# Kernel tuning notes

Hardware: AMD Instinct MI355X
Metric: run time of the kernel (lower is better)

Reference implementation:

```python
import jax, jax.numpy as jnp
import numpy as np

L, D, H, DFF = 4, 1024, 16, 4096
DH = D // H
B, T = 2, 2048
EPS = 1e-5


def setup_inputs() -> dict:
    key = jax.random.key(0)
    ks = jax.random.split(key, 16)
    xav_a = (6.0 / (D + D)) ** 0.5      # xavier_uniform for square DxD
    xav_f1 = (6.0 / (D + DFF)) ** 0.5
    xav_f2 = (6.0 / (DFF + D)) ** 0.5
    def u(k, shape, a):
        return jax.random.uniform(k, shape, jnp.float32, -a, a)
    inp = {
        "x": jax.random.normal(ks[0], (B, T, D), jnp.float32),
        "mask": jnp.ones((B, T), jnp.int32),
        # attention projections, torch Linear layout [out, in]
        "Wq": u(ks[1], (L, D, D), xav_a), "bq": jnp.zeros((L, D), jnp.float32),
        "Wk": u(ks[2], (L, D, D), xav_a), "bk": jnp.zeros((L, D), jnp.float32),
        "Wv": u(ks[3], (L, D, D), xav_a), "bv": jnp.zeros((L, D), jnp.float32),
        "Wo": u(ks[4], (L, D, D), xav_a), "bo": jnp.zeros((L, D), jnp.float32),
        # FFN
        "fc1_w": u(ks[5], (L, DFF, D), xav_f1), "fc1_b": jnp.zeros((L, DFF), jnp.float32),
        "fc2_w": u(ks[6], (L, D, DFF), xav_f2), "fc2_b": jnp.zeros((L, D), jnp.float32),
        # LayerNorms
        "ln1_g": jnp.ones((L, D), jnp.float32), "ln1_b": jnp.zeros((L, D), jnp.float32),
        "ln2_g": jnp.ones((L, D), jnp.float32), "ln2_b": jnp.zeros((L, D), jnp.float32),
        "lnf_g": jnp.ones((D,), jnp.float32), "lnf_b": jnp.zeros((D,), jnp.float32),
    }
    return inp


def _layernorm(x, g, b):
    mu = jnp.mean(x, axis=-1, keepdims=True)
    var = jnp.mean(jnp.square(x - mu), axis=-1, keepdims=True)
    return (x - mu) * jax.lax.rsqrt(var + EPS) * g + b


def _encoder_forward(x, mask, Wq, bq, Wk, bk, Wv, bv, Wo, bo,
                     fc1_w, fc1_b, fc2_w, fc2_b,
                     ln1_g, ln1_b, ln2_g, ln2_b, lnf_g, lnf_b):
    keep = mask.astype(bool)[:, None, None, :]  # [B,1,1,Tk]
    scale = 1.0 / (DH ** 0.5)
    for l in range(L):
        # --- multi-head self-attention ---
        q = (jnp.einsum('btd,ed->bte', x, Wq[l]) + bq[l]).reshape(B, T, H, DH).transpose(0, 2, 1, 3)
        k = (jnp.einsum('btd,ed->bte', x, Wk[l]) + bk[l]).reshape(B, T, H, DH).transpose(0, 2, 1, 3)
        v = (jnp.einsum('btd,ed->bte', x, Wv[l]) + bv[l]).reshape(B, T, H, DH).transpose(0, 2, 1, 3)
        logits = jnp.einsum('bhqd,bhkd->bhqk', q, k) * scale
        logits = jnp.where(keep, logits, -jnp.inf)
        attn = jax.nn.softmax(logits, axis=-1)
        ctx = jnp.einsum('bhqk,bhkd->bhqd', attn, v).transpose(0, 2, 1, 3).reshape(B, T, D)
        attn_out = jnp.einsum('btd,ed->bte', ctx, Wo[l]) + bo[l]
        x = _layernorm(x + attn_out, ln1_g[l], ln1_b[l])
        # --- feed-forward (exact GELU, like torch nn.GELU default) ---
        h = jax.nn.gelu(jnp.einsum('btd,fd->btf', x, fc1_w[l]) + fc1_b[l], approximate=False)
        ff_out = jnp.einsum('btf,df->btd', h, fc2_w[l]) + fc2_b[l]
        x = _layernorm(x + ff_out, ln2_g[l], ln2_b[l])
    return _layernorm(x, lnf_g, lnf_b)


def reference(x, mask, Wq, bq, Wk, bk, Wv, bv, Wo, bo,
              fc1_w, fc1_b, fc2_w, fc2_b,
              ln1_g, ln1_b, ln2_g, ln2_b, lnf_g, lnf_b):
    return _encoder_forward(x, mask, Wq, bq, Wk, bk, Wv, bv, Wo, bo,
                            fc1_w, fc1_b, fc2_w, fc2_b,
                            ln1_g, ln1_b, ln2_g, ln2_b, lnf_g, lnf_b)
```

## Files before the change

kernel.cpp:

```cpp
#include <hip/hip_runtime.h>
#include <hip/hip_bf16.h>
#include <cstdint>

#define BB 2
#define TT 2048
#define DD 1024
#define HH 16
#define DHH 64
#define DFF 4096
#define LL 4
#define MM (BB*TT)
#define NT (TT/64)

typedef __attribute__((ext_vector_type(8))) short short8v;
typedef __attribute__((ext_vector_type(4))) short short4v;
typedef __attribute__((ext_vector_type(4))) float floatx4;

typedef __attribute__((address_space(3))) void lds_void;
typedef const __attribute__((address_space(1))) void glb_void;

__device__ __forceinline__ void gload_lds16(const void* g, void* l) {
  __builtin_amdgcn_global_load_lds((glb_void*)g, (lds_void*)l, 16, 0, 0);
}

__device__ __forceinline__ float bf2f(short s) {
  union { unsigned u; float f; } v; v.u = ((unsigned)(unsigned short)s) << 16; return v.f;
}
__device__ __forceinline__ short f2bf(float f) {
  union { float f; unsigned u; } v; v.f = f;
  unsigned r = (v.u + 0x7fffu + ((v.u >> 16) & 1u)) >> 16;
  return (short)r;
}
__device__ __forceinline__ unsigned pack2bf(float a, float b) {
  __hip_bfloat162 h = __float22bfloat162_rn(make_float2(a, b));
  return *reinterpret_cast<unsigned*>(&h);
}
__device__ __forceinline__ float fexp2(float x) {
  float r; asm("v_exp_f32 %0, %1" : "=v"(r) : "v"(x)); return r;
}
__device__ __forceinline__ float max3f(float a, float b, float c) {
  float r; asm("v_max3_f32 %0, %1, %2, %3" : "=v"(r) : "v"(a), "v"(b), "v"(c)); return r;
}
__device__ __forceinline__ float gelu_fast(float x) {
  const float u = x * x;
  const float w = fmaf(u, -0.10294537f, -2.302203f);
  const float t = fexp2(w * x);
  return x * __builtin_amdgcn_rcpf(1.f + t);
}

#define SCL2 0.18033688011112042f
__device__ __forceinline__ short8v scale8(short8v v) {
  short8v r;
#pragma unroll
  for (int i = 0; i < 8; ++i) r[i] = f2bf(bf2f(v[i]) * SCL2);
  return r;
}

#define SEG (DD*DD)
#define WTOT (4*SEG + 2*DFF*DD)
__global__ __launch_bounds__(256) void cast_layer(
    const float* __restrict__ wq, const float* __restrict__ wk,
    const float* __restrict__ wv, const float* __restrict__ wo,
    const float* __restrict__ f1, const float* __restrict__ f2,
    short* __restrict__ dst)
{
  const int i = (blockIdx.x * 256 + threadIdx.x) * 4;
  const float* src; int off;
  if      (i <     SEG) { src = wq; off = i; }
  else if (i < 2 * SEG) { src = wk; off = i - SEG; }
  else if (i < 3 * SEG) { src = wv; off = i - 2 * SEG; }
  else if (i < 4 * SEG) { src = wo; off = i - 3 * SEG; }
  else if (i < 4 * SEG + DFF * DD) { src = f1; off = i - 4 * SEG; }
  else { src = f2; off = i - 4 * SEG - DFF * DD; }
  const float4 v = *(const float4*)(src + off);
  short4v o; o[0] = f2bf(v.x); o[1] = f2bf(v.y); o[2] = f2bf(v.z); o[3] = f2bf(v.w);
  *(short4v*)(dst + i) = o;
}

__global__ __launch_bounds__(256) void concat_bias(
    const float* __restrict__ a, const float* __restrict__ b,
    const float* __restrict__ c, float* __restrict__ o)
{
  const int i = blockIdx.x * 256 + threadIdx.x;
  o[i] = i < DD ? a[i] : (i < 2 * DD ? b[i - DD] : c[i - 2 * DD]);
}

template<int GELU>
__global__ __launch_bounds__(512, 2) void gemm256(
    const short* __restrict__ A, const short* __restrict__ W,
    const float* __restrict__ bias, short* __restrict__ C,
    int M, int N, int K)
{
  __shared__ __align__(16) short lds[65536];
  const int t = threadIdx.x;
  const int lane = t & 63, wave = t >> 6;
  const int wm = wave >> 2, wn = wave & 3;
  const int l15 = lane & 15, lg = lane >> 4;

  const int nwg = gridDim.x * gridDim.y;
  const int bid0 = blockIdx.y * gridDim.x + blockIdx.x;
  const int q8 = nwg >> 3;
  const int lid = (bid0 & 7) * q8 + (bid0 >> 3);
  const int bx = lid % gridDim.x, by = lid / gridDim.x;

  const size_t abase = (size_t)by * 256 * K;
  const size_t wbase = (size_t)bx * 256 * K;

  floatx4 acc[8][4];
  floatx4 zero = {0.f, 0.f, 0.f, 0.f};
#pragma unroll
  for (int m = 0; m < 8; ++m)
#pragma unroll
    for (int n = 0; n < 4; ++n) acc[m][n] = zero;

#define STG_A(sl_, h_, u_) do {                                                \
    _Pragma("unroll")                                                          \
    for (int j_ = 0; j_ < 2; ++j_) {                                           \
      const int c_ = j_ * 512 + t, r_ = c_ >> 3;                               \
      const int kc_ = (c_ & 7) ^ (r_ & 7);                                     \
      gload_lds16(A + abase + (size_t)((h_) * 128 + r_) * K + (u_) * 64 + kc_ * 8, \
                  &lds[(sl_) * 16384 + (h_) * 8192 + (j_ * 512 + wave * 64) * 8]); \
    } } while (0)
#define STG_B(sl_, h_, u_) do {                                                \
    _Pragma("unroll")                                                          \
    for (int j_ = 0; j_ < 2; ++j_) {                                           \
      const int c_ = j_ * 512 + t, r_ = c_ >> 3;                               \
      const int kc_ = (c_ & 7) ^ (r_ & 7);                                     \
      gload_lds16(W + wbase + (size_t)((h_) * 128 + r_) * K + (u_) * 64 + kc_ * 8, \
                  &lds[32768 + (sl_) * 16384 + (h_) * 8192 + (j_ * 512 + wave * 64) * 8]); \
    } } while (0)

  const int NTK = K >> 6;
  STG_A(0, 0, 0); STG_A(0, 1, 0); STG_B(0, 0, 0); STG_B(0, 1, 0);

  for (int u = 0; u < NTK; ++u) {
    const int sl = u & 1, ns = sl ^ 1;
    const int aoff = sl * 16384 + wm * 8192;
    const int boff = 32768 + sl * 16384 + (wn >> 1) * 8192;
    short8v bfr[4][2];
#pragma unroll
    for (int p = 0; p < 4; ++p) {
      if (p == 0) {
        if (u + 1 < NTK) {
          STG_A(ns, 0, u + 1);
          asm volatile("s_waitcnt vmcnt(2)" ::: "memory");
        } else {
          asm volatile("s_waitcnt vmcnt(0)" ::: "memory");
        }
        __builtin_amdgcn_s_barrier();
#pragma unroll
        for (int n = 0; n < 4; ++n)
#pragma unroll
          for (int kk = 0; kk < 2; ++kk) {
            const int rl = (wn & 1) * 64 + n * 16 + l15;
            bfr[n][kk] = *(const short8v*)&lds[boff + rl * 64 + ((kk * 4 + lg) ^ (rl & 7)) * 8];
          }
      } else if (p == 1) { if (u + 1 < NTK) STG_A(ns, 1, u + 1); }
      else if (p == 2)   { if (u + 1 < NTK) STG_B(ns, 0, u + 1); }
      else               { if (u + 1 < NTK) STG_B(ns, 1, u + 1); }

      short8v af[2][2];
#pragma unroll
      for (int i = 0; i < 2; ++i)
#pragma unroll
        for (int kk = 0; kk < 2; ++kk) {
          const int rl = (2 * p + i) * 16 + l15;
          af[i][kk] = *(const short8v*)&lds[aoff + rl * 64 + ((kk * 4 + lg) ^ (rl & 7)) * 8];
        }
      asm volatile("s_waitcnt lgkmcnt(0)" ::: "memory");
      __builtin_amdgcn_s_setprio(1);
#pragma unroll
      for (int kk = 0; kk < 2; ++kk)
#pragma unroll
        for (int i = 0; i < 2; ++i)
#pragma unroll
          for (int n = 0; n < 4; ++n)
            acc[2 * p + i][n] = __builtin_amdgcn_mfma_f32_16x16x32_bf16(
                af[i][kk], bfr[n][kk], acc[2 * p + i][n], 0, 0, 0);
      __builtin_amdgcn_s_setprio(0);
      __builtin_amdgcn_s_barrier();
    }
  }
#undef STG_A
#undef STG_B

  float bv[4];
#pragma unroll
  for (int n = 0; n < 4; ++n)
    bv[n] = bias[bx * 256 + wn * 64 + n * 16 + l15];
#pragma unroll
  for (int m = 0; m < 8; ++m)
#pragma unroll
    for (int jj = 0; jj < 4; ++jj) {
      const int row = by * 256 + wm * 128 + m * 16 + lg * 4 + jj;
      short* cp = C + (size_t)row * N + bx * 256 + wn * 64 + l15;
#pragma unroll
      for (int n = 0; n < 4; ++n) {
        float v = acc[m][n][jj] + bv[n];
        if (GELU) v = gelu_fast(v);
        cp[n * 16] = f2bf(v);
      }
    }
}

template<int GELU>
__global__ __launch_bounds__(512, 2) void gemm128(
    const short* __restrict__ A, const short* __restrict__ W,
    const float* __restrict__ bias, short* __restrict__ C,
    int M, int N, int K)
{
  __shared__ __align__(16) short lds[32768];
  const int t = threadIdx.x;
  const int lane = t & 63, wave = t >> 6;
  const int wm = wave >> 2, wn = wave & 3;
  const int l15 = lane & 15, lg = lane >> 4;

  const int nwg = gridDim.x * gridDim.y;
  const int bid0 = blockIdx.y * gridDim.x + blockIdx.x;
  const int q8 = nwg >> 3;
  const int lid = (bid0 & 7) * q8 + (bid0 >> 3);
  const int bx = lid % gridDim.x, by = lid / gridDim.x;

  const size_t abase = (size_t)by * 128 * K;
  const size_t wbase = (size_t)bx * 128 * K;

  floatx4 acc[4][2];
  floatx4 zero = {0.f, 0.f, 0.f, 0.f};
#pragma unroll
  for (int m = 0; m < 4; ++m)
#pragma unroll
    for (int n = 0; n < 2; ++n) acc[m][n] = zero;

#define STG_A(sl_, u_) do {                                                    \
    _Pragma("unroll")                                                          \
    for (int j_ = 0; j_ < 2; ++j_) {                                           \
      const int c_ = j_ * 512 + t, r_ = c_ >> 3;                               \
      const int kc_ = (c_ & 7) ^ (r_ & 7);                                     \
      gload_lds16(A + abase + (size_t)r_ * K + (u_) * 64 + kc_ * 8,            \
                  &lds[(sl_) * 8192 + (j_ * 512 + wave * 64) * 8]);            \
    } } while (0)
#define STG_B(sl_, u_) do {                                                    \
    _Pragma("unroll")                                                          \
    for (int j_ = 0; j_ < 2; ++j_) {                                           \
      const int c_ = j_ * 512 + t, r_ = c_ >> 3;                               \
      const int kc_ = (c_ & 7) ^ (r_ & 7);                                     \
      gload_lds16(W + wbase + (size_t)r_ * K + (u_) * 64 + kc_ * 8,            \
                  &lds[16384 + (sl_) * 8192 + (j_ * 512 + wave * 64) * 8]);    \
    } } while (0)

  const int NTK = K >> 6;
  STG_A(0, 0); STG_B(0, 0);

  for (int u = 0; u < NTK; ++u) {
    const int sl = u & 1, ns = sl ^ 1;
    if (u + 1 < NTK) {
      STG_A(ns, u + 1);
      asm volatile("s_waitcnt vmcnt(2)" ::: "memory");
    } else {
      asm volatile("s_waitcnt vmcnt(0)" ::: "memory");
    }
    __builtin_amdgcn_s_barrier();

    short8v bfr[2][2];
#pragma unroll
    for (int n = 0; n < 2; ++n)
#pragma unroll
      for (int kk = 0; kk < 2; ++kk) {
        const int rl = wn * 32 + n * 16 + l15;
        bfr[n][kk] = *(const short8v*)&lds[16384 + sl * 8192 + rl * 64 + ((kk * 4 + lg) ^ (rl & 7)) * 8];
      }
    short8v af0[2][2];
#pragma unroll
    for (int m = 0; m < 2; ++m)
#pragma unroll
      for (int kk = 0; kk < 2; ++kk) {
        const int rl = wm * 64 + m * 16 + l15;
        af0[m][kk] = *(const short8v*)&lds[sl * 8192 + rl * 64 + ((kk * 4 + lg) ^ (rl & 7)) * 8];
      }
    asm volatile("s_waitcnt lgkmcnt(0)" ::: "memory");
    __builtin_amdgcn_s_setprio(1);
#pragma unroll
    for (int kk = 0; kk < 2; ++kk)
#pragma unroll
      for (int m = 0; m < 2; ++m)
#pragma unroll
        for (int n = 0; n < 2; ++n)
          acc[m][n] = __builtin_amdgcn_mfma_f32_16x16x32_bf16(af0[m][kk], bfr[n][kk], acc[m][n], 0, 0, 0);
    __builtin_amdgcn_s_setprio(0);

    if (u + 1 < NTK) STG_B(ns, u + 1);
    short8v af1[2][2];
#pragma unroll
    for (int m = 0; m < 2; ++m)
#pragma unroll
      for (int kk = 0; kk < 2; ++kk) {
        const int rl = wm * 64 + (2 + m) * 16 + l15;
        af1[m][kk] = *(const short8v*)&lds[sl * 8192 + rl * 64 + ((kk * 4 + lg) ^ (rl & 7)) * 8];
      }
    asm volatile("s_waitcnt lgkmcnt(0)" ::: "memory");
    __builtin_amdgcn_s_setprio(1);
#pragma unroll
    for (int kk = 0; kk < 2; ++kk)
#pragma unroll
      for (int m = 0; m < 2; ++m)
#pragma unroll
        for (int n = 0; n < 2; ++n)
          acc[2 + m][n] = __builtin_amdgcn_mfma_f32_16x16x32_bf16(af1[m][kk], bfr[n][kk], acc[2 + m][n], 0, 0, 0);
    __builtin_amdgcn_s_setprio(0);
    __builtin_amdgcn_s_barrier();
  }
#undef STG_A
#undef STG_B

  float bv[2];
#pragma unroll
  for (int n = 0; n < 2; ++n)
    bv[n] = bias[bx * 128 + wn * 32 + n * 16 + l15];
#pragma unroll
  for (int m = 0; m < 4; ++m)
#pragma unroll
    for (int jj = 0; jj < 4; ++jj) {
      const int row = by * 128 + wm * 64 + m * 16 + lg * 4 + jj;
      short* cp = C + (size_t)row * N + bx * 128 + wn * 32 + l15;
#pragma unroll
      for (int n = 0; n < 2; ++n) {
        float v = acc[m][n][jj] + bv[n];
        if (GELU) v = gelu_fast(v);
        cp[n * 16] = f2bf(v);
      }
    }
}

__global__ __launch_bounds__(256) void transpose_v(
    const short* __restrict__ qkv, short* __restrict__ vt)
{
  __shared__ short tile[64][65];
  const int tb = blockIdx.x, h = blockIdx.y, b = blockIdx.z;
  const int t = threadIdx.x;
  const int r = t >> 2, c4 = (t & 3) * 16;
  const short* src = qkv + ((size_t)(b * TT + tb * 64 + r)) * 3072 + 2048 + h * 64 + c4;
#pragma unroll
  for (int i = 0; i < 16; ++i) tile[r][c4 + i] = src[i];
  __syncthreads();
  short* dst = vt + ((size_t)((b * HH + h) * 64 + r)) * TT + tb * 64 + c4;
#pragma unroll
  for (int i = 0; i < 16; ++i) dst[i] = tile[c4 + i][r];
}

#define PSTR 72
__global__ __launch_bounds__(512, 4) void flash_attn(
    const short* __restrict__ qkv, const short* __restrict__ vt,
    const int* __restrict__ mask, short* __restrict__ ctx)
{
  const int t = threadIdx.x;
  const int lane = t & 63, wave = t >> 6;
  const int l15 = lane & 15, lg = lane >> 4;

  const int bid0 = blockIdx.x + gridDim.x * (blockIdx.y + gridDim.y * blockIdx.z);
  const int lid = (bid0 & 7) * 64 + (bid0 >> 3);
  const int qb = lid & 15, h = (lid >> 4) & 15, b = lid >> 8;

  __shared__ __align__(16) short Ks[2][64 * 64];
  __shared__ __align__(16) short Vs[2][64 * 64];
  __shared__ __align__(16) short p_lds[8][16 * PSTR];
  short* prow = p_lds[wave];

  const short* qp = qkv + ((size_t)(b * TT + qb * 128 + wave * 16 + l15)) * 3072 + h * 64;
  const short8v qf0 = scale8(*(const short8v*)(qp + lg * 8));
  const short8v qf1 = scale8(*(const short8v*)(qp + 32 + lg * 8));

  const short* kbase = qkv + (size_t)b * TT * 3072 + 1024 + h * 64;
  const short* vtb   = vt + ((size_t)(b * HH + h)) * 64 * TT;

  const int srow = lane >> 3;
  const int scol = (lane & 7) ^ (srow & 7);

  float m_run = -3e30f, l_run = 0.f;
  floatx4 zero = {0.f, 0.f, 0.f, 0.f};
  floatx4 o[4];
#pragma unroll
  for (int n = 0; n < 4; ++n) o[n] = zero;

#define STAGE_KV(bufi, kb_) do {                                             \
    const int r_ = wave * 8 + srow;                                          \
    gload_lds16(kbase + (size_t)((kb_) * 64 + r_) * 3072 + scol * 8,         \
                &Ks[bufi][wave * 512]);                                      \
    gload_lds16(vtb + (size_t)r_ * TT + (kb_) * 64 + scol * 8,               \
                &Vs[bufi][wave * 512]);                                      \
  } while (0)

  STAGE_KV(0, 0);
  int buf = 0;
  for (int kb = 0; kb < NT; ++kb) {
    if (kb + 1 < NT) {
      STAGE_KV(buf ^ 1, kb + 1);
      asm volatile("s_waitcnt vmcnt(2)" ::: "memory");
    } else {
      asm volatile("s_waitcnt vmcnt(0)" ::: "memory");
    }
    __builtin_amdgcn_s_barrier();

    float cm[4][4];
#pragma unroll
    for (int n = 0; n < 4; ++n) {
      const int4 mv = *(const int4*)&mask[b * TT + kb * 64 + n * 16 + lg * 4];
      cm[n][0] = mv.x ? 0.f : -1.5e30f; cm[n][1] = mv.y ? 0.f : -1.5e30f;
      cm[n][2] = mv.z ? 0.f : -1.5e30f; cm[n][3] = mv.w ? 0.f : -1.5e30f;
    }

    floatx4 s[4];
#pragma unroll
    for (int n = 0; n < 4; ++n) {
      const int row = n * 16 + l15;
      const int ch0 = lg ^ (row & 7);
      const int ch1 = (lg + 4) ^ (row & 7);
      const short8v kf0 = *(const short8v*)&Ks[buf][row * 64 + ch0 * 8];
      const short8v kf1 = *(const short8v*)&Ks[buf][row * 64 + ch1 * 8];
      floatx4 a = zero;
      a = __builtin_amdgcn_mfma_f32_16x16x32_bf16(kf0, qf0, a, 0, 0, 0);
      a = __builtin_amdgcn_mfma_f32_16x16x32_bf16(kf1, qf1, a, 0, 0, 0);
      s[n] = a;
    }
#pragma unroll
    for (int n = 0; n < 4; ++n)
#pragma unroll
      for (int jj = 0; jj < 4; ++jj) s[n][jj] += cm[n][jj];

    const float t0 = max3f(s[0][0], s[0][1], s[0][2]);
    const float t1 = max3f(s[0][3], s[1][0], s[1][1]);
    const float t2 = max3f(s[1][2], s[1][3], s[2][0]);
    const float t3 = max3f(s[2][1], s[2][2], s[2][3]);
    const float t4 = max3f(s[3][0], s[3][1], s[3][2]);
    float mx = fmaxf(max3f(t0, t1, t2), max3f(t3, t4, s[3][3]));
    mx = fmaxf(mx, __shfl_xor(mx, 16, 64));
    mx = fmaxf(mx, __shfl_xor(mx, 32, 64));

    const bool defer = __all(mx - m_run <= 11.5f);
    const float mnew = defer ? m_run : fmaxf(m_run, mx);
    float ps[4];
#pragma unroll
    for (int n = 0; n < 4; ++n) {
      s[n][0] = fexp2(s[n][0] - mnew);
      s[n][1] = fexp2(s[n][1] - mnew);
      s[n][2] = fexp2(s[n][2] - mnew);
      s[n][3] = fexp2(s[n][3] - mnew);
      ps[n] = (s[n][0] + s[n][1]) + (s[n][2] + s[n][3]);
    }
    float sum = (ps[0] + ps[1]) + (ps[2] + ps[3]);
    sum += __shfl_xor(sum, 16, 64);
    sum += __shfl_xor(sum, 32, 64);
    if (defer) {
      l_run += sum;
    } else {
      const float al = fexp2(m_run - mnew);
      l_run = l_run * al + sum;
      m_run = mnew;
      float alo[4];
#pragma unroll
      for (int jj = 0; jj < 4; ++jj) alo[jj] = __shfl(al, lg * 4 + jj, 16);
#pragma unroll
      for (int n = 0; n < 4; ++n)
#pragma unroll
        for (int jj = 0; jj < 4; ++jj) o[n][jj] *= alo[jj];
    }

#pragma unroll
    for (int n = 0; n < 4; ++n) {
      const unsigned u0 = pack2bf(s[n][0], s[n][1]);
      const unsigned u1 = pack2bf(s[n][2], s[n][3]);
      *(uint2*)&prow[l15 * PSTR + n * 16 + lg * 4] = make_uint2(u0, u1);
    }
    const short8v pf0 = *(const short8v*)&prow[l15 * PSTR + lg * 8];
    const short8v pf1 = *(const short8v*)&prow[l15 * PSTR + 32 + lg * 8];

#pragma unroll
    for (int n = 0; n < 4; ++n) {
      const int row = n * 16 + l15;
      const int ch0 = lg ^ (row & 7);
      const int ch1 = (lg + 4) ^ (row & 7);
      const short8v vf0 = *(const short8v*)&Vs[buf][row * 64 + ch0 * 8];
      const short8v vf1 = *(const short8v*)&Vs[buf][row * 64 + ch1 * 8];
      o[n] = __builtin_amdgcn_mfma_f32_16x16x32_bf16(pf0, vf0, o[n], 0, 0, 0);
      o[n] = __builtin_amdgcn_mfma_f32_16x16x32_bf16(pf1, vf1, o[n], 0, 0, 0);
    }
    asm volatile("" ::: "memory");
    __builtin_amdgcn_s_barrier();
    buf ^= 1;
  }
#undef STAGE_KV

#pragma unroll
  for (int jj = 0; jj < 4; ++jj) {
    const float inv = 1.f / __shfl(l_run, lg * 4 + jj, 16);
    const int row = qb * 128 + wave * 16 + lg * 4 + jj;
#pragma unroll
    for (int n = 0; n < 4; ++n)
      ctx[((size_t)(b * TT + row)) * DD + h * 64 + n * 16 + l15] = f2bf(o[n][jj] * inv);
  }
}

__global__ __launch_bounds__(256) void add_ln(
    const float* __restrict__ xres, const short* __restrict__ add,
    const float* __restrict__ g, const float* __restrict__ bb,
    float* __restrict__ outf, short* __restrict__ outb)
{
  const int row = blockIdx.x, t = threadIdx.x;
  const int lane = t & 63, wave = t >> 6;
  const float4 xv = *(const float4*)(xres + (size_t)row * DD + t * 4);
  float y[4] = { xv.x, xv.y, xv.z, xv.w };
  if (add) {
    const short4v av = *(const short4v*)(add + (size_t)row * DD + t * 4);
#pragma unroll
    for (int i = 0; i < 4; ++i) y[i] += bf2f(av[i]);
  }
  float s = y[0] + y[1] + y[2] + y[3];
  float ss = y[0]*y[0] + y[1]*y[1] + y[2]*y[2] + y[3]*y[3];
#pragma unroll
  for (int off = 32; off >= 1; off >>= 1) {
    s  += __shfl_xor(s, off, 64);
    ss += __shfl_xor(ss, off, 64);
  }
  __shared__ float red[2][4];
  if (lane == 0) { red[0][wave] = s; red[1][wave] = ss; }
  __syncthreads();
  s  = red[0][0] + red[0][1] + red[0][2] + red[0][3];
  ss = red[1][0] + red[1][1] + red[1][2] + red[1][3];
  const float mu = s * (1.f / DD);
  const float var = ss * (1.f / DD) - mu * mu;
  const float rs = rsqrtf(var + 1e-5f);
  const float4 gv = *(const float4*)(g + t * 4);
  const float4 bv = *(const float4*)(bb + t * 4);
  float o[4];
  o[0] = (y[0] - mu) * rs * gv.x + bv.x;
  o[1] = (y[1] - mu) * rs * gv.y + bv.y;
  o[2] = (y[2] - mu) * rs * gv.z + bv.z;
  o[3] = (y[3] - mu) * rs * gv.w + bv.w;
  if (outf) *(float4*)(outf + (size_t)row * DD + t * 4) = make_float4(o[0], o[1], o[2], o[3]);
  if (outb) {
    short4v ov;
#pragma unroll
    for (int i = 0; i < 4; ++i) ov[i] = f2bf(o[i]);
    *(short4v*)(outb + (size_t)row * DD + t * 4) = ov;
  }
}

__global__ __launch_bounds__(256) void cast_in(
    const float* __restrict__ x, float* __restrict__ xf,
    short* __restrict__ xb)
{
  const int i = (blockIdx.x * 256 + threadIdx.x) * 4;
  const float4 v = *(const float4*)(x + i);
  *(float4*)(xf + i) = v;
  short4v o; o[0] = f2bf(v.x); o[1] = f2bf(v.y); o[2] = f2bf(v.z); o[3] = f2bf(v.w);
  *(short4v*)(xb + i) = o;
}

extern "C" void kernel_launch(void* const* d_in, const int* in_sizes, int n_in,
                              void* d_out, int out_size, void* d_ws, size_t ws_size,
                              hipStream_t stream) {
  const float* x   = (const float*)d_in[0];
  const int* mask  = (const int*)d_in[1];
  const float* Wq  = (const float*)d_in[2];
  const float* bq  = (const float*)d_in[3];
  const float* Wk  = (const float*)d_in[4];
  const float* bk  = (const float*)d_in[5];
  const float* Wv  = (const float*)d_in[6];
  const float* bv  = (const float*)d_in[7];
  const float* Wo  = (const float*)d_in[8];
  const float* bo  = (const float*)d_in[9];
  const float* f1w = (const float*)d_in[10];
  const float* f1b = (const float*)d_in[11];
  const float* f2w = (const float*)d_in[12];
  const float* f2b = (const float*)d_in[13];
  const float* l1g = (const float*)d_in[14];
  const float* l1b = (const float*)d_in[15];
  const float* l2g = (const float*)d_in[16];
  const float* l2b = (const float*)d_in[17];
  const float* lfg = (const float*)d_in[18];
  const float* lfb = (const float*)d_in[19];
  float* out = (float*)d_out;

  char* ws = (char*)d_ws;
  const size_t MB = 1u << 20;
  float* xf   = (float*)(ws);
  short* xb   = (short*)(ws + 16 * MB);
  short* qkv  = (short*)(ws + 24 * MB);
  short* vt_  = (short*)(ws + 48 * MB);
  short* ctx  = (short*)(ws + 56 * MB);
  short* tmp  = (short*)(ws + 64 * MB);
  float* fbias= (float*)(ws + 64 * MB);
  short* wbuf = (short*)(ws + 72 * MB);
  short* hb   = qkv;

  cast_in<<<(MM * DD) / (256 * 4), 256, 0, stream>>>(x, xf, xb);

  for (int l = 0; l < LL; ++l) {
    cast_layer<<<WTOT / (256 * 4), 256, 0, stream>>>(
        Wq + (size_t)l * SEG, Wk + (size_t)l * SEG, Wv + (size_t)l * SEG, Wo + (size_t)l * SEG,
        f1w + (size_t)l * DFF * DD, f2w + (size_t)l * DD * DFF, wbuf);
    concat_bias<<<12, 256, 0, stream>>>(bq + l * DD, bk + l * DD, bv + l * DD, fbias);
    const short* wqkv_b = wbuf;
    const short* wo_b   = wbuf + 3 * SEG;
    const short* f1_b   = wbuf + 4 * SEG;
    const short* f2_b   = wbuf + 4 * SEG + DFF * DD;

    gemm256<0><<<dim3(3072 / 256, MM / 256), 512, 0, stream>>>(xb, wqkv_b, fbias, qkv, MM, 3072, DD);
    transpose_v<<<dim3(TT / 64, HH, BB), 256, 0, stream>>>(qkv, vt_);
    flash_attn<<<dim3(TT / 128, HH, BB), 512, 0, stream>>>(qkv, vt_, mask, ctx);
    gemm128<0><<<dim3(DD / 128, MM / 128), 512, 0, stream>>>(ctx, wo_b, bo + l * DD, tmp, MM, DD, DD);
    add_ln<<<MM, 256, 0, stream>>>(xf, tmp, l1g + l * DD, l1b + l * DD, xf, xb);
    gemm256<1><<<dim3(DFF / 256, MM / 256), 512, 0, stream>>>(xb, f1_b, f1b + l * DFF, hb, MM, DFF, DD);
    gemm128<0><<<dim3(DD / 128, MM / 128), 512, 0, stream>>>(hb, f2_b, f2b + l * DD, tmp, MM, DD, DFF);
    add_ln<<<MM, 256, 0, stream>>>(xf, tmp, l2g + l * DD, l2b + l * DD, xf, xb);
  }
  add_ln<<<MM, 256, 0, stream>>>(xf, nullptr, lfg, lfb, out, nullptr);
}
```

Measured before the change: 958.0 us.

## Triple-buffer gemm128 and flash-attn K/V staging; fold QKV bias concat into GEMM

The 128-tile GEMM and the flash-attention K/V loop move from double to triple LDS buffering. Loads run two tiles ahead, the trailing barrier per iteration is removed, and A and W for a tile are staged together. The QKV GEMM now picks among the three bias vectors by column segment, so the concat_bias launch per layer is gone. This trades more LDS per block, which may lower occupancy, for better overlap of global loads with MFMA work and fewer barriers.

```diff
diff --git a/kernel.cpp b/kernel.cpp
--- a/kernel.cpp
+++ b/kernel.cpp
@@ -77,18 +77,11 @@
   *(short4v*)(dst + i) = o;
 }
 
-__global__ __launch_bounds__(256) void concat_bias(
-    const float* __restrict__ a, const float* __restrict__ b,
-    const float* __restrict__ c, float* __restrict__ o)
-{
-  const int i = blockIdx.x * 256 + threadIdx.x;
-  o[i] = i < DD ? a[i] : (i < 2 * DD ? b[i - DD] : c[i - 2 * DD]);
-}
-
-template<int GELU>
+template<int GELU, int QKV>
 __global__ __launch_bounds__(512, 2) void gemm256(
     const short* __restrict__ A, const short* __restrict__ W,
-    const float* __restrict__ bias, short* __restrict__ C,
+    const float* __restrict__ b0, const float* __restrict__ b1,
+    const float* __restrict__ b2, short* __restrict__ C,
     int M, int N, int K)
 {
   __shared__ __align__(16) short lds[65536];
@@ -184,10 +177,19 @@
 #undef STG_A
 #undef STG_B
 
+  const float* bp;
+  int cbase = bx * 256 + wn * 64;
+  if (QKV) {
+    const int seg = cbase >> 10;
+    bp = (seg == 0) ? b0 : (seg == 1 ? b1 : b2);
+    cbase -= seg << 10;
+  } else {
+    bp = b0;
+  }
   float bv[4];
 #pragma unroll
   for (int n = 0; n < 4; ++n)
-    bv[n] = bias[bx * 256 + wn * 64 + n * 16 + l15];
+    bv[n] = bp[cbase + n * 16 + l15];
 #pragma unroll
   for (int m = 0; m < 8; ++m)
 #pragma unroll
@@ -209,7 +211,7 @@
     const float* __restrict__ bias, short* __restrict__ C,
     int M, int N, int K)
 {
-  __shared__ __align__(16) short lds[32768];
+  __shared__ __align__(16) short lds[49152];
   const int t = threadIdx.x;
   const int lane = t & 63, wave = t >> 6;
   const int wm = wave >> 2, wn = wave & 3;
@@ -231,86 +233,55 @@
 #pragma unroll
     for (int n = 0; n < 2; ++n) acc[m][n] = zero;
 
-#define STG_A(sl_, u_) do {                                                    \
+#define STG128(sl_, u_) do {                                                   \
     _Pragma("unroll")                                                          \
     for (int j_ = 0; j_ < 2; ++j_) {                                           \
       const int c_ = j_ * 512 + t, r_ = c_ >> 3;                               \
       const int kc_ = (c_ & 7) ^ (r_ & 7);                                     \
       gload_lds16(A + abase + (size_t)r_ * K + (u_) * 64 + kc_ * 8,            \
                   &lds[(sl_) * 8192 + (j_ * 512 + wave * 64) * 8]);            \
+      gload_lds16(W + wbase + (size_t)r_ * K + (u_) * 64 + kc_ * 8,            \
+                  &lds[24576 + (sl_) * 8192 + (j_ * 512 + wave * 64) * 8]);    \
     } } while (0)
-#define STG_B(sl_, u_) do {                                                    \
-    _Pragma("unroll")                                                          \
-    for (int j_ = 0; j_ < 2; ++j_) {                                           \
-      const int c_ = j_ * 512 + t, r_ = c_ >> 3;                               \
-      const int kc_ = (c_ & 7) ^ (r_ & 7);                                     \
-      gload_lds16(W + wbase + (size_t)r_ * K + (u_) * 64 + kc_ * 8,            \
-                  &lds[16384 + (sl_) * 8192 + (j_ * 512 + wave * 64) * 8]);    \
-    } } while (0)
 
   const int NTK = K >> 6;
-  STG_A(0, 0); STG_B(0, 0);
+  STG128(0, 0);
+  STG128(1, 1);
 
   for (int u = 0; u < NTK; ++u) {
-    const int sl = u & 1, ns = sl ^ 1;
-    if (u + 1 < NTK) {
-      STG_A(ns, u + 1);
-      asm volatile("s_waitcnt vmcnt(2)" ::: "memory");
-    } else {
-      asm volatile("s_waitcnt vmcnt(0)" ::: "memory");
-    }
+    const int sl = u % 3;
+    if (u + 1 < NTK) asm volatile("s_waitcnt vmcnt(4)" ::: "memory");
+    else             asm volatile("s_waitcnt vmcnt(0)" ::: "memory");
     __builtin_amdgcn_s_barrier();
-
-    short8v bfr[2][2];
+    if (u + 2 < NTK) STG128((u + 2) % 3, u + 2);
+
+    short8v bfr[2][2], af[4][2];
 #pragma unroll
     for (int n = 0; n < 2; ++n)
 #pragma unroll
       for (int kk = 0; kk < 2; ++kk) {
         const int rl = wn * 32 + n * 16 + l15;
-        bfr[n][kk] = *(const short8v*)&lds[16384 + sl * 8192 + rl * 64 + ((kk * 4 + lg) ^ (rl & 7)) * 8];
+        bfr[n][kk] = *(const short8v*)&lds[24576 + sl * 8192 + rl * 64 + ((kk * 4 + lg) ^ (rl & 7)) * 8];
       }
-    short8v af0[2][2];
-#pragma unroll
-    for (int m = 0; m < 2; ++m)
+#pragma unroll
+    for (int m = 0; m < 4; ++m)
 #pragma unroll
       for (int kk = 0; kk < 2; ++kk) {
-        const int rl = wm * 64 + m * 16 + l15;
-        af0[m][kk] = *(const short8v*)&lds[sl * 8192 + rl * 64 + ((kk * 4 + lg) ^ (rl & 7)) * 8];
+        const int rl = wm * 32 + ((m & 1) * 16) + l15 + (m >> 1) * 64;
+        af[m][kk] = *(const short8v*)&lds[sl * 8192 + rl * 64 + ((kk * 4 + lg) ^ (rl & 7)) * 8];
       }
     asm volatile("s_waitcnt lgkmcnt(0)" ::: "memory");
     __builtin_amdgcn_s_setprio(1);
 #pragma unroll
     for (int kk = 0; kk < 2; ++kk)
 #pragma unroll
-      for (int m = 0; m < 2; ++m)
+      for (int m = 0; m < 4; ++m)
 #pragma unroll
         for (int n = 0; n < 2; ++n)
-          acc[m][n] = __builtin_amdgcn_mfma_f32_16x16x32_bf16(af0[m][kk], bfr[n][kk], acc[m][n], 0, 0, 0);
+          acc[m][n] = __builtin_amdgcn_mfma_f32_16x16x32_bf16(af[m][kk], bfr[n][kk], acc[m][n], 0, 0, 0);
     __builtin_amdgcn_s_setprio(0);
-
-    if (u + 1 < NTK) STG_B(ns, u + 1);
-    short8v af1[2][2];
-#pragma unroll
-    for (int m = 0; m < 2; ++m)
-#pragma unroll
-      for (int kk = 0; kk < 2; ++kk) {
-        const int rl = wm * 64 + (2 + m) * 16 + l15;
-        af1[m][kk] = *(const short8v*)&lds[sl * 8192 + rl * 64 + ((kk * 4 + lg) ^ (rl & 7)) * 8];
-      }
-    asm volatile("s_waitcnt lgkmcnt(0)" ::: "memory");
-    __builtin_amdgcn_s_setprio(1);
-#pragma unroll
-    for (int kk = 0; kk < 2; ++kk)
-#pragma unroll
-      for (int m = 0; m < 2; ++m)
-#pragma unroll
-        for (int n = 0; n < 2; ++n)
-          acc[2 + m][n] = __builtin_amdgcn_mfma_f32_16x16x32_bf16(af1[m][kk], bfr[n][kk], acc[2 + m][n], 0, 0, 0);
-    __builtin_amdgcn_s_setprio(0);
-    __builtin_amdgcn_s_barrier();
-  }
-#undef STG_A
-#undef STG_B
+  }
+#undef STG128
 
   float bv[2];
 #pragma unroll
@@ -320,7 +291,7 @@
   for (int m = 0; m < 4; ++m)
 #pragma unroll
     for (int jj = 0; jj < 4; ++jj) {
-      const int row = by * 128 + wm * 64 + m * 16 + lg * 4 + jj;
+      const int row = by * 128 + wm * 32 + (m & 1) * 16 + (m >> 1) * 64 + lg * 4 + jj;
       short* cp = C + (size_t)row * N + bx * 128 + wn * 32 + l15;
 #pragma unroll
       for (int n = 0; n < 2; ++n) {
@@ -360,8 +331,8 @@
   const int lid = (bid0 & 7) * 64 + (bid0 >> 3);
   const int qb = lid & 15, h = (lid >> 4) & 15, b = lid >> 8;
 
-  __shared__ __align__(16) short Ks[2][64 * 64];
-  __shared__ __align__(16) short Vs[2][64 * 64];
+  __shared__ __align__(16) short Ks[3][64 * 64];
+  __shared__ __align__(16) short Vs[3][64 * 64];
   __shared__ __align__(16) short p_lds[8][16 * PSTR];
   short* prow = p_lds[wave];
 
@@ -390,15 +361,13 @@
   } while (0)
 
   STAGE_KV(0, 0);
-  int buf = 0;
+  STAGE_KV(1, 1);
   for (int kb = 0; kb < NT; ++kb) {
-    if (kb + 1 < NT) {
-      STAGE_KV(buf ^ 1, kb + 1);
-      asm volatile("s_waitcnt vmcnt(2)" ::: "memory");
-    } else {
-      asm volatile("s_waitcnt vmcnt(0)" ::: "memory");
-    }
+    const int sl = kb % 3;
+    if (kb + 1 < NT) asm volatile("s_waitcnt vmcnt(2)" ::: "memory");
+    else             asm volatile("s_waitcnt vmcnt(0)" ::: "memory");
     __builtin_amdgcn_s_barrier();
+    if (kb + 2 < NT) STAGE_KV((kb + 2) % 3, kb + 2);
 
     float cm[4][4];
 #pragma unroll
@@ -414,8 +383,8 @@
       const int row = n * 16 + l15;
       const int ch0 = lg ^ (row & 7);
       const int ch1 = (lg + 4) ^ (row & 7);
-      const short8v kf0 = *(const short8v*)&Ks[buf][row * 64 + ch0 * 8];
-      const short8v kf1 = *(const short8v*)&Ks[buf][row * 64 + ch1 * 8];
+      const short8v kf0 = *(const short8v*)&Ks[sl][row * 64 + ch0 * 8];
+      const short8v kf1 = *(const short8v*)&Ks[sl][row * 64 + ch1 * 8];
       floatx4 a = zero;
       a = __builtin_amdgcn_mfma_f32_16x16x32_bf16(kf0, qf0, a, 0, 0, 0);
       a = __builtin_amdgcn_mfma_f32_16x16x32_bf16(kf1, qf1, a, 0, 0, 0);
@@ -478,14 +447,11 @@
       const int row = n * 16 + l15;
       const int ch0 = lg ^ (row & 7);
       const int ch1 = (lg + 4) ^ (row & 7);
-      const short8v vf0 = *(const short8v*)&Vs[buf][row * 64 + ch0 * 8];
-      const short8v vf1 = *(const short8v*)&Vs[buf][row * 64 + ch1 * 8];
+      const short8v vf0 = *(const short8v*)&Vs[sl][row * 64 + ch0 * 8];
+      const short8v vf1 = *(const short8v*)&Vs[sl][row * 64 + ch1 * 8];
       o[n] = __builtin_amdgcn_mfma_f32_16x16x32_bf16(pf0, vf0, o[n], 0, 0, 0);
       o[n] = __builtin_amdgcn_mfma_f32_16x16x32_bf16(pf1, vf1, o[n], 0, 0, 0);
     }
-    asm volatile("" ::: "memory");
-    __builtin_amdgcn_s_barrier();
-    buf ^= 1;
   }
 #undef STAGE_KV
 
@@ -588,7 +554,6 @@
   short* vt_  = (short*)(ws + 48 * MB);
   short* ctx  = (short*)(ws + 56 * MB);
   short* tmp  = (short*)(ws + 64 * MB);
-  float* fbias= (float*)(ws + 64 * MB);
   short* wbuf = (short*)(ws + 72 * MB);
   short* hb   = qkv;
 
@@ -598,18 +563,19 @@
     cast_layer<<<WTOT / (256 * 4), 256, 0, stream>>>(
         Wq + (size_t)l * SEG, Wk + (size_t)l * SEG, Wv + (size_t)l * SEG, Wo + (size_t)l * SEG,
         f1w + (size_t)l * DFF * DD, f2w + (size_t)l * DD * DFF, wbuf);
-    concat_bias<<<12, 256, 0, stream>>>(bq + l * DD, bk + l * DD, bv + l * DD, fbias);
     const short* wqkv_b = wbuf;
     const short* wo_b   = wbuf + 3 * SEG;
     const short* f1_b   = wbuf + 4 * SEG;
     const short* f2_b   = wbuf + 4 * SEG + DFF * DD;
 
-    gemm256<0><<<dim3(3072 / 256, MM / 256), 512, 0, stream>>>(xb, wqkv_b, fbias, qkv, MM, 3072, DD);
+    gemm256<0,1><<<dim3(3072 / 256, MM / 256), 512, 0, stream>>>(
+        xb, wqkv_b, bq + l * DD, bk + l * DD, bv + l * DD, qkv, MM, 3072, DD);
     transpose_v<<<dim3(TT / 64, HH, BB), 256, 0, stream>>>(qkv, vt_);
     flash_attn<<<dim3(TT / 128, HH, BB), 512, 0, stream>>>(qkv, vt_, mask, ctx);
     gemm128<0><<<dim3(DD / 128, MM / 128), 512, 0, stream>>>(ctx, wo_b, bo + l * DD, tmp, MM, DD, DD);
     add_ln<<<MM, 256, 0, stream>>>(xf, tmp, l1g + l * DD, l1b + l * DD, xf, xb);
-    gemm256<1><<<dim3(DFF / 256, MM / 256), 512, 0, stream>>>(xb, f1_b, f1b + l * DFF, hb, MM, DFF, DD);
+    gemm256<1,0><<<dim3(DFF / 256, MM / 256), 512, 0, stream>>>(
+        xb, f1_b, f1b + l * DFF, nullptr, nullptr, hb, MM, DFF, DD);
     gemm128<0><<<dim3(DD / 128, MM / 128), 512, 0, stream>>>(hb, f2_b, f2b + l * DD, tmp, MM, DD, DFF);
     add_ln<<<MM, 256, 0, stream>>>(xf, tmp, l2g + l * DD, l2b + l * DD, xf, xb);
   }
```

Result: no change. 941.5 us (-1.7%).
